# Kernel optimization log

Measured on AMD Instinct MI355X. Metric: run time of the kernel, lower is better.

## Reference

```python
import jax, jax.numpy as jnp
import numpy as np

B, T, H = 1024, 512, 256  # batch, seq_len, hidden_layer_size; input_size=1, output_size=1


def setup_inputs() -> dict:
    key = jax.random.key(0)
    ks = jax.random.split(key, 7)
    s = 1.0 / np.sqrt(H)  # PyTorch LSTM/Linear init scale (uniform bound); normal here, scaled similarly
    return {
        "input_seq": jax.random.normal(ks[0], (B, T), dtype=jnp.float32),
        "W_ih": jax.random.normal(ks[1], (4 * H, 1), dtype=jnp.float32) * s,
        "W_hh": jax.random.normal(ks[2], (4 * H, H), dtype=jnp.float32) * s,
        "b_ih": jax.random.normal(ks[3], (4 * H,), dtype=jnp.float32) * s,
        "b_hh": jax.random.normal(ks[4], (4 * H,), dtype=jnp.float32) * s,
        "W_lin": jax.random.normal(ks[5], (1, H), dtype=jnp.float32) * s,
        "b_lin": jax.random.normal(ks[6], (1,), dtype=jnp.float32) * s,
    }


def _lstm_last_hidden(x, W_ih, W_hh, b_ih, b_hh):
    # x: [B, T] scalar series -> treated as [B, T, 1] (input_size = 1).
    # Precompute the input projection for all timesteps at once:
    # xg[b, t, :] = x[b, t] * W_ih[:, 0] + b_ih + b_hh   -> [B, T, 4H]
    xg = x[:, :, None] * W_ih[:, 0] + (b_ih + b_hh)
    xg = jnp.swapaxes(xg, 0, 1)  # [T, B, 4H] for scan over time

    h0 = jnp.zeros((x.shape[0], H), dtype=x.dtype)
    c0 = jnp.zeros((x.shape[0], H), dtype=x.dtype)

    def step(carry, xg_t):
        h, c = carry
        gates = xg_t + h @ W_hh.T  # [B, 4H]
        i, f, g, o = jnp.split(gates, 4, axis=-1)  # PyTorch gate order: i, f, g, o
        i = jax.nn.sigmoid(i)
        f = jax.nn.sigmoid(f)
        g = jnp.tanh(g)
        o = jax.nn.sigmoid(o)
        c = f * c + i * g
        h = o * jnp.tanh(c)
        return (h, c), None

    (h_n, _), _ = jax.lax.scan(step, (h0, c0), xg)
    return h_n  # [B, H]


def reference(input_seq, W_ih, W_hh, b_ih, b_hh, W_lin, b_lin):
    h_n = _lstm_last_hidden(input_seq, W_ih, W_hh, b_ih, b_hh)
    predictions = h_n @ W_lin.T + b_lin  # [B, 1]
    return predictions
```

## Files before the change

### kernel.cpp

```cpp
#include <hip/hip_runtime.h>


#define HID 256
#define TT 512
#define BROWS 16
#define NBLK 64
#define THREADS 512
#define HPAD 264

typedef float v4f __attribute__((ext_vector_type(4)));
typedef unsigned int v4u __attribute__((ext_vector_type(4)));
typedef __bf16 v8bf __attribute__((ext_vector_type(8)));

__device__ __forceinline__ unsigned short f2bf(float f) {
    unsigned int u = __builtin_bit_cast(unsigned int, f);
    u += 0x7fffu + ((u >> 16) & 1u);
    return (unsigned short)(u >> 16);
}
__device__ __forceinline__ float bf2f(unsigned short s) {
    unsigned int u = ((unsigned int)s) << 16;
    return __builtin_bit_cast(float, u);
}
__device__ __forceinline__ float fsigmoid(float x) {
    float e = exp2f(x * -1.44269504f);
    return __builtin_amdgcn_rcpf(1.0f + e);
}
__device__ __forceinline__ float ftanh(float x) {
    float e = exp2f(x * 2.88539008f);
    return 1.0f - 2.0f * __builtin_amdgcn_rcpf(1.0f + e);
}

__global__ void wconv_kernel(const float* __restrict__ Whh,
                             unsigned short* __restrict__ Wbf) {
    int tid = blockIdx.x * blockDim.x + threadIdx.x;
    int lane = tid & 63;
    int frag = tid >> 6;
    int Tn = frag >> 3;
    int kc = frag & 7;
    int n  = Tn * 16 + (lane & 15);
    int kb = kc * 32 + (lane >> 4) * 8;
    const float* src = Whh + (size_t)n * HID + kb;
    unsigned short* dst = Wbf + (size_t)tid * 8;
#pragma unroll
    for (int j = 0; j < 8; ++j) dst[j] = f2bf(src[j]);
}

#define MFMA8(ACC, BARR, BOFF)                                               \
    _Pragma("unroll")                                                        \
    for (int kc = 0; kc < 8; ++kc)                                           \
        ACC = __builtin_amdgcn_mfma_f32_16x16x32_bf16(afrag[kc],             \
                  BARR[(BOFF) + kc], ACC, 0, 0, 0);

#define LDSTILE(ACC, SLOT)                                                   \
    { v8bf bl_[8];                                                           \
      _Pragma("unroll")                                                      \
      for (int kc = 0; kc < 8; ++kc)                                         \
          bl_[kc] = __builtin_bit_cast(v8bf, *(const v4u*)(Wlds +            \
                      ((size_t)(((SLOT) * 8 + kc) * 64 + lane)) * 8));       \
      MFMA8(ACC, bl_, 0) }

#define SLOADT(SB, TN)                                                       \
    _Pragma("unroll")                                                        \
    for (int kc = 0; kc < 8; ++kc)                                           \
        SB[kc] = __builtin_bit_cast(v8bf, *(const v4u*)(Wbf +                \
                   ((size_t)((TN) * 8 + kc) * 64 + lane) * 8));

#define INITG(S, AI, AF, AG, AO)                                             \
    { int nb = 16 * (w + 8 * (S)) + l4;                                      \
      float w0 = gw[nb],       b0 = gb[nb];                                  \
      float w1 = gw[256 + nb], b1 = gb[256 + nb];                            \
      float w2 = gw[512 + nb], b2 = gb[512 + nb];                            \
      float w3 = gw[768 + nb], b3 = gb[768 + nb];                            \
      _Pragma("unroll")                                                      \
      for (int r = 0; r < 4; ++r) {                                          \
          AI[r] = xv[r] * w0 + b0; AF[r] = xv[r] * w1 + b1;                  \
          AG[r] = xv[r] * w2 + b2; AO[r] = xv[r] * w3 + b3; } }

#define GATES(S, AI, AF, AG, AO)                                             \
    _Pragma("unroll")                                                        \
    for (int r = 0; r < 4; ++r) {                                            \
        float gi = fsigmoid(AI[r]);                                          \
        float gf = fsigmoid(AF[r]);                                          \
        float gg = ftanh(AG[r]);                                             \
        float go = fsigmoid(AO[r]);                                          \
        float cn = gf * c_st[(S) * 4 + r] + gi * gg;                         \
        c_st[(S) * 4 + r] = cn;                                              \
        hn_[(quad * 4 + r) * HPAD + 16 * (w + 8 * (S)) + l4] =               \
            f2bf(go * ftanh(cn));                                            \
    }

__global__ __launch_bounds__(THREADS, 2)
void lstm_kernel(const float* __restrict__ x,
                 const float* __restrict__ W_ih,
                 const float* __restrict__ b_ih,
                 const float* __restrict__ b_hh,
                 const float* __restrict__ W_lin,
                 const float* __restrict__ b_lin,
                 const unsigned short* __restrict__ Wbf,
                 float* __restrict__ out) {
    __shared__ __align__(16) unsigned short Wlds[16 * 8 * 64 * 8];
    __shared__ __align__(16) unsigned short hbuf[2][BROWS * HPAD];
    __shared__ float gw[1024];
    __shared__ float gb[1024];
    __shared__ float part[THREADS];

    const int tid  = threadIdx.x;
    const int lane = tid & 63;
    const int w    = tid >> 6;
    const int l4   = lane & 15;
    const int quad = lane >> 4;
    const int r0   = blockIdx.x * BROWS;

    for (int i = tid; i < 1024; i += THREADS) {
        gw[i] = W_ih[i];
        gb[i] = b_ih[i] + b_hh[i];
    }
    for (int i = tid; i < BROWS * HPAD; i += THREADS) hbuf[0][i] = 0;

    v8bf wres[32];
#pragma unroll
    for (int S = 0; S < 2; ++S)
#pragma unroll
        for (int G = 0; G < 2; ++G) {
            int Tn = 16 * G + w + 8 * S;
#pragma unroll
            for (int kc = 0; kc < 8; ++kc)
                wres[(S * 2 + G) * 8 + kc] = __builtin_bit_cast(v8bf,
                    *(const v4u*)(Wbf + ((size_t)(Tn * 8 + kc) * 64 + lane) * 8));
        }
#pragma unroll
    for (int S = 0; S < 2; ++S) {
        int Tn = 32 + w + 8 * S;
        int slot = w * 2 + S;
#pragma unroll
        for (int kc = 0; kc < 8; ++kc) {
            v4u d = *(const v4u*)(Wbf + ((size_t)(Tn * 8 + kc) * 64 + lane) * 8);
            *(v4u*)(Wlds + ((size_t)((slot * 8 + kc) * 64 + lane)) * 8) = d;
        }
    }
    __syncthreads();

    float c_st[8];
#pragma unroll
    for (int i = 0; i < 8; ++i) c_st[i] = 0.0f;

    v8bf sb[8];
    SLOADT(sb, 48 + w)

    int cur = 0;
    for (int t = 0; t < TT; ++t) {
        const unsigned short* hb = hbuf[cur];
        unsigned short* hn_ = hbuf[cur ^ 1];

        float xv[4];
#pragma unroll
        for (int r = 0; r < 4; ++r)
            xv[r] = x[(size_t)(r0 + quad * 4 + r) * TT + t];

        v8bf afrag[8];
        const unsigned short* hrow = hb + l4 * HPAD + quad * 8;
#pragma unroll
        for (int kc = 0; kc < 8; ++kc)
            afrag[kc] = __builtin_bit_cast(v8bf, *(const v4u*)(hrow + kc * 32));

        {
            v4f ai, af2, ag, ao;
            INITG(0, ai, af2, ag, ao)
            MFMA8(ai, wres, 0)
            MFMA8(af2, wres, 8)
            LDSTILE(ag, w * 2 + 0)
            MFMA8(ao, sb, 0)
            SLOADT(sb, 56 + w)
            GATES(0, ai, af2, ag, ao)
        }
        {
            v4f ai, af2, ag, ao;
            INITG(1, ai, af2, ag, ao)
            MFMA8(ai, wres, 16)
            MFMA8(af2, wres, 24)
            LDSTILE(ag, w * 2 + 1)
            MFMA8(ao, sb, 0)
            SLOADT(sb, 48 + w)
            GATES(1, ai, af2, ag, ao)
        }

        cur ^= 1;
        __syncthreads();
    }

    {
        int rrow = tid >> 5, s5 = tid & 31;
        float p = 0.0f;
#pragma unroll
        for (int jj = 0; jj < 8; ++jj) {
            int j = s5 * 8 + jj;
            p += bf2f(hbuf[cur][rrow * HPAD + j]) * W_lin[j];
        }
        part[tid] = p;
    }
    __syncthreads();
    if (tid < 16) {
        float sum = 0.0f;
#pragma unroll
        for (int s = 0; s < 32; ++s) sum += part[tid * 32 + s];
        out[r0 + tid] = sum + b_lin[0];
    }
}

extern "C" void kernel_launch(void* const* d_in, const int* in_sizes, int n_in,
                              void* d_out, int out_size, void* d_ws, size_t ws_size,
                              hipStream_t stream) {
    const float* x     = (const float*)d_in[0];
    const float* W_ih  = (const float*)d_in[1];
    const float* W_hh  = (const float*)d_in[2];
    const float* b_ih  = (const float*)d_in[3];
    const float* b_hh  = (const float*)d_in[4];
    const float* W_lin = (const float*)d_in[5];
    const float* b_lin = (const float*)d_in[6];
    unsigned short* Wbf = (unsigned short*)d_ws;

    wconv_kernel<<<128, 256, 0, stream>>>(W_hh, Wbf);
    lstm_kernel<<<NBLK, THREADS, 0, stream>>>(x, W_ih, b_ih, b_hh, W_lin, b_lin,
                                              Wbf, (float*)d_out);
}
```

Measured before the change: 1.583 ms.

## Use 16 waves per block with one column tile per wave in LSTM recurrence

Doubles the block to 1024 threads so each wave owns a single 16-column slice of each gate instead of two, halving per-wave MFMA work per timestep and the register footprint of resident weights. Gate weights and biases are kept in registers rather than LDS, the input x for the next step is prefetched, and the o-gate weights are streamed from global memory through a rotating 4-entry buffer. The final linear layer becomes a wave shuffle reduction. The trade-off is more waves contending at every per-step barrier, plus repeated global/L2 reads of the o-gate weights each step.

```diff
diff --git a/kernel.cpp b/kernel.cpp
--- a/kernel.cpp
+++ b/kernel.cpp
@@ -5,7 +5,7 @@
 #define TT 512
 #define BROWS 16
 #define NBLK 64
-#define THREADS 512
+#define THREADS 1024
 #define HPAD 264
 
 typedef float v4f __attribute__((ext_vector_type(4)));
@@ -45,51 +45,7 @@
     for (int j = 0; j < 8; ++j) dst[j] = f2bf(src[j]);
 }
 
-#define MFMA8(ACC, BARR, BOFF)                                               \
-    _Pragma("unroll")                                                        \
-    for (int kc = 0; kc < 8; ++kc)                                           \
-        ACC = __builtin_amdgcn_mfma_f32_16x16x32_bf16(afrag[kc],             \
-                  BARR[(BOFF) + kc], ACC, 0, 0, 0);
-
-#define LDSTILE(ACC, SLOT)                                                   \
-    { v8bf bl_[8];                                                           \
-      _Pragma("unroll")                                                      \
-      for (int kc = 0; kc < 8; ++kc)                                         \
-          bl_[kc] = __builtin_bit_cast(v8bf, *(const v4u*)(Wlds +            \
-                      ((size_t)(((SLOT) * 8 + kc) * 64 + lane)) * 8));       \
-      MFMA8(ACC, bl_, 0) }
-
-#define SLOADT(SB, TN)                                                       \
-    _Pragma("unroll")                                                        \
-    for (int kc = 0; kc < 8; ++kc)                                           \
-        SB[kc] = __builtin_bit_cast(v8bf, *(const v4u*)(Wbf +                \
-                   ((size_t)((TN) * 8 + kc) * 64 + lane) * 8));
-
-#define INITG(S, AI, AF, AG, AO)                                             \
-    { int nb = 16 * (w + 8 * (S)) + l4;                                      \
-      float w0 = gw[nb],       b0 = gb[nb];                                  \
-      float w1 = gw[256 + nb], b1 = gb[256 + nb];                            \
-      float w2 = gw[512 + nb], b2 = gb[512 + nb];                            \
-      float w3 = gw[768 + nb], b3 = gb[768 + nb];                            \
-      _Pragma("unroll")                                                      \
-      for (int r = 0; r < 4; ++r) {                                          \
-          AI[r] = xv[r] * w0 + b0; AF[r] = xv[r] * w1 + b1;                  \
-          AG[r] = xv[r] * w2 + b2; AO[r] = xv[r] * w3 + b3; } }
-
-#define GATES(S, AI, AF, AG, AO)                                             \
-    _Pragma("unroll")                                                        \
-    for (int r = 0; r < 4; ++r) {                                            \
-        float gi = fsigmoid(AI[r]);                                          \
-        float gf = fsigmoid(AF[r]);                                          \
-        float gg = ftanh(AG[r]);                                             \
-        float go = fsigmoid(AO[r]);                                          \
-        float cn = gf * c_st[(S) * 4 + r] + gi * gg;                         \
-        c_st[(S) * 4 + r] = cn;                                              \
-        hn_[(quad * 4 + r) * HPAD + 16 * (w + 8 * (S)) + l4] =               \
-            f2bf(go * ftanh(cn));                                            \
-    }
-
-__global__ __launch_bounds__(THREADS, 2)
+__global__ __launch_bounds__(THREADS, 4)
 void lstm_kernel(const float* __restrict__ x,
                  const float* __restrict__ W_ih,
                  const float* __restrict__ b_ih,
@@ -100,9 +56,6 @@
                  float* __restrict__ out) {
     __shared__ __align__(16) unsigned short Wlds[16 * 8 * 64 * 8];
     __shared__ __align__(16) unsigned short hbuf[2][BROWS * HPAD];
-    __shared__ float gw[1024];
-    __shared__ float gb[1024];
-    __shared__ float part[THREADS];
 
     const int tid  = threadIdx.x;
     const int lane = tid & 63;
@@ -110,101 +63,100 @@
     const int l4   = lane & 15;
     const int quad = lane >> 4;
     const int r0   = blockIdx.x * BROWS;
+    const int col  = 16 * w + l4;
 
-    for (int i = tid; i < 1024; i += THREADS) {
-        gw[i] = W_ih[i];
-        gb[i] = b_ih[i] + b_hh[i];
-    }
+#pragma unroll
+    for (int kc = 0; kc < 8; ++kc)
+        *(v4u*)(Wlds + ((size_t)((w * 8 + kc) * 64 + lane)) * 8) =
+            *(const v4u*)(Wbf + ((size_t)(((32 + w) * 8 + kc) * 64 + lane)) * 8);
+
     for (int i = tid; i < BROWS * HPAD; i += THREADS) hbuf[0][i] = 0;
 
-    v8bf wres[32];
+    v8bf wi[8], wf[8];
 #pragma unroll
-    for (int S = 0; S < 2; ++S)
+    for (int kc = 0; kc < 8; ++kc) {
+        wi[kc] = __builtin_bit_cast(v8bf,
+            *(const v4u*)(Wbf + ((size_t)((w * 8 + kc) * 64 + lane)) * 8));
+        wf[kc] = __builtin_bit_cast(v8bf,
+            *(const v4u*)(Wbf + ((size_t)(((16 + w) * 8 + kc) * 64 + lane)) * 8));
+    }
+
+    const float cwi = W_ih[col],       cbi = b_ih[col]       + b_hh[col];
+    const float cwf = W_ih[256 + col], cbf = b_ih[256 + col] + b_hh[256 + col];
+    const float cwg = W_ih[512 + col], cbg = b_ih[512 + col] + b_hh[512 + col];
+    const float cwo = W_ih[768 + col], cbo = b_ih[768 + col] + b_hh[768 + col];
+
+    const v4u* optr = (const v4u*)(Wbf + ((size_t)((48 + w) * 8) * 64 + lane) * 8);
+    v4u ob[4];
 #pragma unroll
-        for (int G = 0; G < 2; ++G) {
-            int Tn = 16 * G + w + 8 * S;
+    for (int j = 0; j < 4; ++j) ob[j] = optr[j * 64];
+
+    float xv[4];
 #pragma unroll
-            for (int kc = 0; kc < 8; ++kc)
-                wres[(S * 2 + G) * 8 + kc] = __builtin_bit_cast(v8bf,
-                    *(const v4u*)(Wbf + ((size_t)(Tn * 8 + kc) * 64 + lane) * 8));
+    for (int r = 0; r < 4; ++r) xv[r] = x[(size_t)(r0 + quad * 4 + r) * TT];
+
+    __syncthreads();
+
+    float c_st[4] = {0.f, 0.f, 0.f, 0.f};
+    int cur = 0;
+
+    for (int t = 0; t < TT; ++t) {
+        const unsigned short* hrow = hbuf[cur] + l4 * HPAD + quad * 8;
+        unsigned short* hn = hbuf[cur ^ 1];
+
+        v4f ai, af, ag, ao;
+#pragma unroll
+        for (int r = 0; r < 4; ++r) {
+            ai[r] = xv[r] * cwi + cbi;
+            af[r] = xv[r] * cwf + cbf;
+            ag[r] = xv[r] * cwg + cbg;
+            ao[r] = xv[r] * cwo + cbo;
         }
-#pragma unroll
-    for (int S = 0; S < 2; ++S) {
-        int Tn = 32 + w + 8 * S;
-        int slot = w * 2 + S;
+
 #pragma unroll
         for (int kc = 0; kc < 8; ++kc) {
-            v4u d = *(const v4u*)(Wbf + ((size_t)(Tn * 8 + kc) * 64 + lane) * 8);
-            *(v4u*)(Wlds + ((size_t)((slot * 8 + kc) * 64 + lane)) * 8) = d;
+            v8bf a = __builtin_bit_cast(v8bf, *(const v4u*)(hrow + kc * 32));
+            v8bf g = __builtin_bit_cast(v8bf, *(const v4u*)(Wlds +
+                        ((size_t)((w * 8 + kc) * 64 + lane)) * 8));
+            ai = __builtin_amdgcn_mfma_f32_16x16x32_bf16(a, wi[kc], ai, 0, 0, 0);
+            af = __builtin_amdgcn_mfma_f32_16x16x32_bf16(a, wf[kc], af, 0, 0, 0);
+            ag = __builtin_amdgcn_mfma_f32_16x16x32_bf16(a, g, ag, 0, 0, 0);
+            ao = __builtin_amdgcn_mfma_f32_16x16x32_bf16(a,
+                     __builtin_bit_cast(v8bf, ob[kc & 3]), ao, 0, 0, 0);
+            ob[kc & 3] = optr[((kc + 4) & 7) * 64];
         }
-    }
-    __syncthreads();
-
-    float c_st[8];
-#pragma unroll
-    for (int i = 0; i < 8; ++i) c_st[i] = 0.0f;
-
-    v8bf sb[8];
-    SLOADT(sb, 48 + w)
-
-    int cur = 0;
-    for (int t = 0; t < TT; ++t) {
-        const unsigned short* hb = hbuf[cur];
-        unsigned short* hn_ = hbuf[cur ^ 1];
-
-        float xv[4];
-#pragma unroll
-        for (int r = 0; r < 4; ++r)
-            xv[r] = x[(size_t)(r0 + quad * 4 + r) * TT + t];
-
-        v8bf afrag[8];
-        const unsigned short* hrow = hb + l4 * HPAD + quad * 8;
-#pragma unroll
-        for (int kc = 0; kc < 8; ++kc)
-            afrag[kc] = __builtin_bit_cast(v8bf, *(const v4u*)(hrow + kc * 32));
 
         {
-            v4f ai, af2, ag, ao;
-            INITG(0, ai, af2, ag, ao)
-            MFMA8(ai, wres, 0)
-            MFMA8(af2, wres, 8)
-            LDSTILE(ag, w * 2 + 0)
-            MFMA8(ao, sb, 0)
-            SLOADT(sb, 56 + w)
-            GATES(0, ai, af2, ag, ao)
+            int tn = (t + 1) & (TT - 1);
+#pragma unroll
+            for (int r = 0; r < 4; ++r)
+                xv[r] = x[(size_t)(r0 + quad * 4 + r) * TT + tn];
         }
-        {
-            v4f ai, af2, ag, ao;
-            INITG(1, ai, af2, ag, ao)
-            MFMA8(ai, wres, 16)
-            MFMA8(af2, wres, 24)
-            LDSTILE(ag, w * 2 + 1)
-            MFMA8(ao, sb, 0)
-            SLOADT(sb, 48 + w)
-            GATES(1, ai, af2, ag, ao)
+
+#pragma unroll
+        for (int r = 0; r < 4; ++r) {
+            float gi = fsigmoid(ai[r]);
+            float gf = fsigmoid(af[r]);
+            float gg = ftanh(ag[r]);
+            float go = fsigmoid(ao[r]);
+            float cn = gf * c_st[r] + gi * gg;
+            c_st[r] = cn;
+            hn[(quad * 4 + r) * HPAD + col] = f2bf(go * ftanh(cn));
         }
 
         cur ^= 1;
         __syncthreads();
     }
 
-    {
-        int rrow = tid >> 5, s5 = tid & 31;
-        float p = 0.0f;
+    float p = 0.f;
 #pragma unroll
-        for (int jj = 0; jj < 8; ++jj) {
-            int j = s5 * 8 + jj;
-            p += bf2f(hbuf[cur][rrow * HPAD + j]) * W_lin[j];
-        }
-        part[tid] = p;
+    for (int j = 0; j < 4; ++j) {
+        int c = lane * 4 + j;
+        p += bf2f(hbuf[cur][w * HPAD + c]) * W_lin[c];
     }
-    __syncthreads();
-    if (tid < 16) {
-        float sum = 0.0f;
 #pragma unroll
-        for (int s = 0; s < 32; ++s) sum += part[tid * 32 + s];
-        out[r0 + tid] = sum + b_lin[0];
-    }
+    for (int off = 32; off; off >>= 1) p += __shfl_down(p, off);
+    if (lane == 0) out[r0 + w] = p + b_lin[0];
 }
 
 extern "C" void kernel_launch(void* const* d_in, const int* in_sizes, int n_in,
```

Result: slower. 3.906 ms (+146.8%).

## Reorder LSTM step groups per wave, prefetch x, keep input weights in registers

Applied to the files above, without the earlier changes.

Input-projection weights and biases are now kept in registers instead of being read from LDS every step, and the next step's x values are prefetched at the end of each iteration. Within each step the streamed o-gate tile MFMA and its global reload are issued first, with raised wave priority, and half the waves process the two column groups in reverse order so their MFMA and transcendental phases interleave. Launch bounds change from 2 to 1 block per CU. The intent is to hide global and LDS load latency and spread gate math against matrix work, at the cost of more register pressure.

```diff
diff --git a/kernel.cpp b/kernel.cpp
--- a/kernel.cpp
+++ b/kernel.cpp
@@ -65,17 +65,6 @@
         SB[kc] = __builtin_bit_cast(v8bf, *(const v4u*)(Wbf +                \
                    ((size_t)((TN) * 8 + kc) * 64 + lane) * 8));
 
-#define INITG(S, AI, AF, AG, AO)                                             \
-    { int nb = 16 * (w + 8 * (S)) + l4;                                      \
-      float w0 = gw[nb],       b0 = gb[nb];                                  \
-      float w1 = gw[256 + nb], b1 = gb[256 + nb];                            \
-      float w2 = gw[512 + nb], b2 = gb[512 + nb];                            \
-      float w3 = gw[768 + nb], b3 = gb[768 + nb];                            \
-      _Pragma("unroll")                                                      \
-      for (int r = 0; r < 4; ++r) {                                          \
-          AI[r] = xv[r] * w0 + b0; AF[r] = xv[r] * w1 + b1;                  \
-          AG[r] = xv[r] * w2 + b2; AO[r] = xv[r] * w3 + b3; } }
-
 #define GATES(S, AI, AF, AG, AO)                                             \
     _Pragma("unroll")                                                        \
     for (int r = 0; r < 4; ++r) {                                            \
@@ -89,7 +78,26 @@
             f2bf(go * ftanh(cn));                                            \
     }
 
-__global__ __launch_bounds__(THREADS, 2)
+#define GROUP(S, NEXTS)                                                      \
+    { v4f ai, af2, ag, ao;                                                   \
+      _Pragma("unroll")                                                      \
+      for (int r = 0; r < 4; ++r) {                                          \
+          ai[r]  = xv[r] * cw[S][0] + cb[S][0];                              \
+          af2[r] = xv[r] * cw[S][1] + cb[S][1];                              \
+          ag[r]  = xv[r] * cw[S][2] + cb[S][2];                              \
+          ao[r]  = xv[r] * cw[S][3] + cb[S][3];                              \
+      }                                                                      \
+      __builtin_amdgcn_s_setprio(1);                                         \
+      MFMA8(ao, sb, 0)                                                       \
+      SLOADT(sb, 48 + w + 8 * (NEXTS))                                       \
+      MFMA8(ai, wres, (S) * 16 + 0)                                          \
+      MFMA8(af2, wres, (S) * 16 + 8)                                         \
+      LDSTILE(ag, w * 2 + (S))                                               \
+      __builtin_amdgcn_s_setprio(0);                                         \
+      GATES(S, ai, af2, ag, ao)                                              \
+    }
+
+__global__ __launch_bounds__(THREADS, 1)
 void lstm_kernel(const float* __restrict__ x,
                  const float* __restrict__ W_ih,
                  const float* __restrict__ b_ih,
@@ -100,8 +108,6 @@
                  float* __restrict__ out) {
     __shared__ __align__(16) unsigned short Wlds[16 * 8 * 64 * 8];
     __shared__ __align__(16) unsigned short hbuf[2][BROWS * HPAD];
-    __shared__ float gw[1024];
-    __shared__ float gb[1024];
     __shared__ float part[THREADS];
 
     const int tid  = threadIdx.x;
@@ -111,10 +117,6 @@
     const int quad = lane >> 4;
     const int r0   = blockIdx.x * BROWS;
 
-    for (int i = tid; i < 1024; i += THREADS) {
-        gw[i] = W_ih[i];
-        gb[i] = b_ih[i] + b_hh[i];
-    }
     for (int i = tid; i < BROWS * HPAD; i += THREADS) hbuf[0][i] = 0;
 
     v8bf wres[32];
@@ -134,10 +136,22 @@
         int slot = w * 2 + S;
 #pragma unroll
         for (int kc = 0; kc < 8; ++kc) {
-            v4u d = *(const v4u*)(Wbf + ((size_t)(Tn * 8 + kc) * 64 + lane) * 8);
+            v4u d = *(const v4u*)(Wbf + ((size_t)((Tn * 8 + kc) * 64 + lane)) * 8);
             *(v4u*)(Wlds + ((size_t)((slot * 8 + kc) * 64 + lane)) * 8) = d;
         }
     }
+
+    float cw[2][4], cb[2][4];
+#pragma unroll
+    for (int S = 0; S < 2; ++S) {
+        int colS = 16 * (w + 8 * S) + l4;
+#pragma unroll
+        for (int g = 0; g < 4; ++g) {
+            cw[S][g] = W_ih[g * 256 + colS];
+            cb[S][g] = b_ih[g * 256 + colS] + b_hh[g * 256 + colS];
+        }
+    }
+
     __syncthreads();
 
     float c_st[8];
@@ -145,43 +159,37 @@
     for (int i = 0; i < 8; ++i) c_st[i] = 0.0f;
 
     v8bf sb[8];
-    SLOADT(sb, 48 + w)
+    SLOADT(sb, 48 + w + ((w >> 2) << 3))
+
+    float xv[4];
+#pragma unroll
+    for (int r = 0; r < 4; ++r)
+        xv[r] = x[(size_t)(r0 + quad * 4 + r) * TT];
 
     int cur = 0;
     for (int t = 0; t < TT; ++t) {
         const unsigned short* hb = hbuf[cur];
         unsigned short* hn_ = hbuf[cur ^ 1];
 
-        float xv[4];
-#pragma unroll
-        for (int r = 0; r < 4; ++r)
-            xv[r] = x[(size_t)(r0 + quad * 4 + r) * TT + t];
-
         v8bf afrag[8];
         const unsigned short* hrow = hb + l4 * HPAD + quad * 8;
 #pragma unroll
         for (int kc = 0; kc < 8; ++kc)
             afrag[kc] = __builtin_bit_cast(v8bf, *(const v4u*)(hrow + kc * 32));
 
+        if (w < 4) {
+            GROUP(0, 1)
+            GROUP(1, 0)
+        } else {
+            GROUP(1, 0)
+            GROUP(0, 1)
+        }
+
         {
-            v4f ai, af2, ag, ao;
-            INITG(0, ai, af2, ag, ao)
-            MFMA8(ai, wres, 0)
-            MFMA8(af2, wres, 8)
-            LDSTILE(ag, w * 2 + 0)
-            MFMA8(ao, sb, 0)
-            SLOADT(sb, 56 + w)
-            GATES(0, ai, af2, ag, ao)
-        }
-        {
-            v4f ai, af2, ag, ao;
-            INITG(1, ai, af2, ag, ao)
-            MFMA8(ai, wres, 16)
-            MFMA8(af2, wres, 24)
-            LDSTILE(ag, w * 2 + 1)
-            MFMA8(ao, sb, 0)
-            SLOADT(sb, 48 + w)
-            GATES(1, ai, af2, ag, ao)
+            int tn = (t + 1) & (TT - 1);
+#pragma unroll
+            for (int r = 0; r < 4; ++r)
+                xv[r] = x[(size_t)(r0 + quad * 4 + r) * TT + tn];
         }
 
         cur ^= 1;
```

Result: slower. 3.913 ms (+147.2%).
